# Optimization experiments

Measured on AMD Instinct MI355X. Metric: run time of the kernel, lower is better.

## Reference

```python
import jax, jax.numpy as jnp
import numpy as np
import math

SCALE = math.sqrt(256.0)

def setup_inputs() -> dict:
    key = jax.random.key(0)
    k1, k2, k3, k4, k5 = jax.random.split(key, 5)
    B, C, T, D = 8, 80, 2048, 256
    bound = 1.0 / math.sqrt(C)
    x = jax.random.normal(k1, (B, C, T), dtype=jnp.float32)
    Wk = jax.random.uniform(k2, (D, C), minval=-bound, maxval=bound, dtype=jnp.float32)
    bk = jax.random.uniform(k3, (D,), minval=-bound, maxval=bound, dtype=jnp.float32)
    Wq = jax.random.uniform(k4, (D, C), minval=-bound, maxval=bound, dtype=jnp.float32)
    bq = jax.random.uniform(k5, (D,), minval=-bound, maxval=bound, dtype=jnp.float32)
    return {"x": x, "Wk": Wk, "bk": bk, "Wq": Wq, "bq": bq}

def reference(x, Wk, bk, Wq, bq):
    # x: [B, C=80, T]; work in time-major layout [B, T, C]
    xt = jnp.swapaxes(x, 1, 2)                      # [B, T, C]
    K = xt @ Wk.T + bk                              # [B, T, 256]
    Q = xt @ Wq.T + bq                              # [B, T, 256]
    # softmax over last dim (dim=2 in torch) of K Q^T / sqrt(256)
    att = jax.nn.softmax(jnp.einsum('bid,bjd->bij', K, Q) / SCALE, axis=2)
    # original per-timestep loop is exactly att @ xt (values = raw input, no V proj)
    out = jnp.einsum('bij,bjc->bic', att, xt)       # [B, T, C]
    return jnp.swapaxes(out, 1, 2)                  # [B, C, T]
```

## Files before the change

kernel.cpp:

```cpp
#include <hip/hip_runtime.h>
#include <hip/hip_bf16.h>
#include <math.h>

typedef __bf16 bf16;
typedef __bf16 bf16x8 __attribute__((ext_vector_type(8)));
typedef float  f32x4  __attribute__((ext_vector_type(4)));
typedef float  f32x16 __attribute__((ext_vector_type(16)));
typedef uint32_t u32x2 __attribute__((ext_vector_type(2)));
typedef uint32_t u32x4 __attribute__((ext_vector_type(4)));

#define MFMA16(a, b, c) __builtin_amdgcn_mfma_f32_16x16x32_bf16((a), (b), (c), 0, 0, 0)
#define MFMA32(a, b, c) __builtin_amdgcn_mfma_f32_32x32x16_bf16((a), (b), (c), 0, 0, 0)

typedef const uint32_t __attribute__((address_space(1)))* gq_t;
typedef uint32_t __attribute__((address_space(3)))* lq_t;

constexpr int B_ = 8, C_ = 80, T_ = 2048, D_ = 256;
constexpr int NS = 4;
constexpr float LOG2E_16 = 0.090169989f;

static __device__ inline uint32_t pkbf(float lo, float hi) {
  bf16 l = (bf16)lo, h = (bf16)hi;
  uint16_t lb = __builtin_bit_cast(uint16_t, l), hb = __builtin_bit_cast(uint16_t, h);
  return (uint32_t)lb | ((uint32_t)hb << 16);
}

constexpr int VF_TILE = 3 * 2 * 2 * 32 * 8;

__global__ __launch_bounds__(256) void wconv_kernel(
    const float* __restrict__ Wk, const float* __restrict__ bk,
    const float* __restrict__ Wq, const float* __restrict__ bq,
    bf16* __restrict__ Wbf)
{
  const int mat = blockIdx.x, c8 = blockIdx.y, d = threadIdx.x;
  const float* W    = mat ? Wq : Wk;
  const float* bias = mat ? bq : bk;
  bf16x8 o;
  #pragma unroll
  for (int e = 0; e < 8; ++e) {
    int c = c8 * 8 + e;
    float v = (c < 80) ? W[d * C_ + c] : (c == 80 ? bias[d] : 0.f);
    o[e] = (bf16)v;
  }
  *reinterpret_cast<bf16x8*>(Wbf + (size_t)(mat * 256 + d) * 96 + c8 * 8) = o;
}

__global__ __launch_bounds__(256) void proj_kernel(
    const float* __restrict__ x,
    const bf16* __restrict__ Wbf,
    bf16* __restrict__ Kb,
    bf16* __restrict__ Qb,
    bf16* __restrict__ Vf)
{
  const int t0   = blockIdx.x * 32;
  const int b    = blockIdx.y;
  const int mat  = blockIdx.z;
  const int tid  = threadIdx.x;
  const int w    = tid >> 6;
  const int lane = tid & 63;
  const int h    = lane >> 4;
  const int lr   = lane & 15;

  const float* xb = x + (size_t)b * C_ * T_;

  if (mat == 0) {
    bf16* vout = Vf + (size_t)(b * 64 + blockIdx.x) * VF_TILE;
    #pragma unroll
    for (int g = 0; g < 2; ++g) {
      int f = tid + g * 256;
      if (f < 384) {
        int il2 = f & 31, hi2 = (f >> 5) & 1, kj2 = (f >> 6) & 1, cb2 = f >> 7;
        int c = cb2 * 32 + il2;
        bf16x8 o;
        if (c < 80) {
          const float* sp = xb + (size_t)c * T_ + t0 + kj2 * 16 + hi2 * 8;
          f32x4 v0 = *reinterpret_cast<const f32x4*>(sp);
          f32x4 v1 = *reinterpret_cast<const f32x4*>(sp + 4);
          #pragma unroll
          for (int e = 0; e < 4; ++e) { o[e] = (bf16)v0[e]; o[e + 4] = (bf16)v1[e]; }
        } else {
          #pragma unroll
          for (int e = 0; e < 8; ++e) o[e] = (bf16)0.f;
        }
        *reinterpret_cast<bf16x8*>(vout + f * 8) = o;
      }
    }
  }

  bf16x8 afrag[2][3];
  #pragma unroll
  for (int ib = 0; ib < 2; ++ib) {
    int t = t0 + ib * 16 + lr;
    #pragma unroll
    for (int ks = 0; ks < 3; ++ks) {
      bf16x8 v;
      #pragma unroll
      for (int e = 0; e < 8; ++e) {
        int c = ks * 32 + h * 8 + e;
        float val;
        if (c < 80)       val = xb[c * T_ + t];
        else if (c == 80) val = 1.0f;
        else              val = 0.0f;
        v[e] = (bf16)val;
      }
      afrag[ib][ks] = v;
    }
  }

  const int nb0 = w * 4;
  bf16* outp = mat ? Qb : Kb;

  f32x4 acc[2][4];
  #pragma unroll
  for (int ib = 0; ib < 2; ++ib)
    #pragma unroll
    for (int nb = 0; nb < 4; ++nb)
      acc[ib][nb] = f32x4{0.f, 0.f, 0.f, 0.f};

  #pragma unroll
  for (int nb = 0; nb < 4; ++nb) {
    int d = (nb0 + nb) * 16 + lr;
    const bf16* wrow = Wbf + (size_t)(mat * 256 + d) * 96;
    #pragma unroll
    for (int ks = 0; ks < 3; ++ks) {
      bf16x8 bv = *reinterpret_cast<const bf16x8*>(wrow + ks * 32 + h * 8);
      #pragma unroll
      for (int ib = 0; ib < 2; ++ib)
        acc[ib][nb] = MFMA16(afrag[ib][ks], bv, acc[ib][nb]);
    }
  }

  #pragma unroll
  for (int ib = 0; ib < 2; ++ib)
    #pragma unroll
    for (int nb = 0; nb < 4; ++nb) {
      int d = (nb0 + nb) * 16 + lr;
      #pragma unroll
      for (int r = 0; r < 4; ++r) {
        int t = t0 + ib * 16 + h * 4 + r;
        outp[(size_t)(b * T_ + t) * D_ + d] = (bf16)acc[ib][nb][r];
      }
    }
}

__global__ __launch_bounds__(256, 2) void attn_kernel(
    const bf16* __restrict__ Kb,
    const bf16* __restrict__ Qb,
    const bf16* __restrict__ Vf,
    float* __restrict__ Opart,
    float* __restrict__ mpart,
    float* __restrict__ lpart)
{
  constexpr int BN = 64, NSTG = T_ / BN;
  constexpr int STG_PER = NSTG / NS;
  __shared__ bf16 qlds[2][BN * D_];

  const int flat = blockIdx.x;
  const int b    = flat & 7;
  const int rem  = flat >> 3;
  const int it   = rem & 15;
  const int s    = rem >> 4;
  const int i0   = it * 128;

  const int tid  = threadIdx.x;
  const int w    = tid >> 6;
  const int lane = tid & 63;
  const int il   = lane & 31;
  const int hi   = lane >> 5;
  const int iw   = i0 + w * 32;

  const bf16* Kbase = Kb + (size_t)b * T_ * D_;
  const bf16* Qbase = Qb + (size_t)b * T_ * D_;
  const bf16* Vbase = Vf + (size_t)b * 64 * VF_TILE;

  bf16x8 kf[16];
  {
    const bf16* kp = Kbase + (size_t)(iw + il) * D_ + hi * 8;
    #pragma unroll
    for (int ks = 0; ks < 16; ++ks)
      kf[ks] = *reinterpret_cast<const bf16x8*>(kp + ks * 16);
  }

  f32x16 oacc[3];
  #pragma unroll
  for (int cb = 0; cb < 3; ++cb)
    #pragma unroll
    for (int r = 0; r < 16; ++r) oacc[cb][r] = 0.f;
  float m_run = -INFINITY, l_run = 0.f;

  const int st0 = s * STG_PER;
  const int off = (it & 3) * 2;
  auto smap = [&](int t) { return st0 + ((t - st0 + off) & (STG_PER - 1)); };

  auto stage = [&](int st, int buf) {
    #pragma unroll
    for (int q = 0; q < 8; ++q) {
      int f = tid + 256 * q;
      int j = f >> 5, c = f & 31;
      const bf16* src = Qbase + (size_t)(st * BN + j) * D_ + ((c ^ (j & 31)) << 3);
      __builtin_amdgcn_global_load_lds((gq_t)src,
          (lq_t)&qlds[buf][(q * 256 + w * 64) * 8], 16, 0, 0);
    }
  };

  stage(smap(st0), 0);
  asm volatile("s_waitcnt vmcnt(0)" ::: "memory");
  __syncthreads();

  int cur = 0;
  for (int t = st0; t < st0 + STG_PER; ++t, cur ^= 1) {
    const int st = smap(t);
    if (t + 1 < st0 + STG_PER) stage(smap(t + 1), cur ^ 1);

    #pragma unroll
    for (int hf = 0; hf < 2; ++hf) {
      const int j32 = st * 2 + hf;

      const bf16* vt = Vbase + (size_t)j32 * VF_TILE + lane * 8;
      bf16x8 vf[3][2];
      #pragma unroll
      for (int cb = 0; cb < 3; ++cb)
        #pragma unroll
        for (int kj = 0; kj < 2; ++kj)
          vf[cb][kj] = *reinterpret_cast<const bf16x8*>(vt + (cb * 2 + kj) * 512);

      f32x16 sacc;
      #pragma unroll
      for (int r = 0; r < 16; ++r) sacc[r] = 0.f;
      __builtin_amdgcn_s_setprio(1);
      #pragma unroll
      for (int ks = 0; ks < 16; ++ks) {
        bf16x8 qa = *reinterpret_cast<const bf16x8*>(
            &qlds[cur][(hf * 32 + il) * 256 + (((hi + 2 * ks) ^ il) << 3)]);
        sacc = MFMA32(qa, kf[ks], sacc);
      }
      __builtin_amdgcn_s_setprio(0);

      float p16[16];
      #pragma unroll
      for (int r = 0; r < 16; ++r) p16[r] = sacc[r];
      float q0 = fmaxf(fmaxf(p16[0],  p16[1]),  p16[2]);
      float q1 = fmaxf(fmaxf(p16[3],  p16[4]),  p16[5]);
      float q2 = fmaxf(fmaxf(p16[6],  p16[7]),  p16[8]);
      float q3 = fmaxf(fmaxf(p16[9],  p16[10]), p16[11]);
      float q4 = fmaxf(fmaxf(p16[12], p16[13]), p16[14]);
      float mx = fmaxf(fmaxf(fmaxf(q0, q1), q2),
                       fmaxf(fmaxf(q3, q4), p16[15]));
      mx = fmaxf(mx, __shfl_xor(mx, 32));

      if (!__all(mx <= m_run + 48.f)) {
        float mnew  = fmaxf(m_run, mx);
        float alpha = exp2f((m_run - mnew) * LOG2E_16);
        m_run = mnew;
        l_run *= alpha;
        #pragma unroll
        for (int cb = 0; cb < 3; ++cb)
          #pragma unroll
          for (int r = 0; r < 16; ++r) oacc[cb][r] *= alpha;
      }
      #pragma unroll
      for (int r = 0; r < 16; ++r)
        p16[r] = exp2f((p16[r] - m_run) * LOG2E_16);
      {
        float s0 = (p16[0] + p16[1]) + (p16[2] + p16[3]);
        float s1 = (p16[4] + p16[5]) + (p16[6] + p16[7]);
        float s2 = (p16[8] + p16[9]) + (p16[10] + p16[11]);
        float s3 = (p16[12] + p16[13]) + (p16[14] + p16[15]);
        l_run += (s0 + s1) + (s2 + s3);
      }

      uint32_t a0 = pkbf(p16[0],  p16[1]),  a1 = pkbf(p16[2],  p16[3]);
      uint32_t c0 = pkbf(p16[4],  p16[5]),  c1 = pkbf(p16[6],  p16[7]);
      uint32_t a2 = pkbf(p16[8],  p16[9]),  a3 = pkbf(p16[10], p16[11]);
      uint32_t c2 = pkbf(p16[12], p16[13]), c3 = pkbf(p16[14], p16[15]);
      u32x2 w0 = __builtin_amdgcn_permlane32_swap(a0, c0, false, false);
      u32x2 w1 = __builtin_amdgcn_permlane32_swap(a1, c1, false, false);
      u32x2 w2 = __builtin_amdgcn_permlane32_swap(a2, c2, false, false);
      u32x2 w3 = __builtin_amdgcn_permlane32_swap(a3, c3, false, false);
      u32x4 pb0 = { w0[0], w1[0], w0[1], w1[1] };
      u32x4 pb1 = { w2[0], w3[0], w2[1], w3[1] };
      bf16x8 pbf0 = __builtin_bit_cast(bf16x8, pb0);
      bf16x8 pbf1 = __builtin_bit_cast(bf16x8, pb1);

      __builtin_amdgcn_s_setprio(1);
      #pragma unroll
      for (int cb = 0; cb < 3; ++cb) {
        oacc[cb] = MFMA32(vf[cb][0], pbf0, oacc[cb]);
        oacc[cb] = MFMA32(vf[cb][1], pbf1, oacc[cb]);
      }
      __builtin_amdgcn_s_setprio(0);
    }

    asm volatile("s_waitcnt vmcnt(0)" ::: "memory");
    __syncthreads();
  }

  l_run += __shfl_xor(l_run, 32);

  float* ob = Opart + (size_t)(s * B_ + b) * C_ * T_;
  #pragma unroll
  for (int cb = 0; cb < 3; ++cb)
    #pragma unroll
    for (int r = 0; r < 16; ++r) {
      if (cb < 2 || r < 8) {
        int c = cb * 32 + (r & 3) + 8 * (r >> 2) + 4 * hi;
        ob[(size_t)c * T_ + iw + il] = oacc[cb][r];
      }
    }
  if (lane < 32) {
    mpart[(size_t)(s * B_ + b) * T_ + iw + il] = m_run;
    lpart[(size_t)(s * B_ + b) * T_ + iw + il] = l_run;
  }
}

__global__ __launch_bounds__(256) void merge_kernel(
    const float* __restrict__ Opart,
    const float* __restrict__ mpart,
    const float* __restrict__ lpart,
    float* __restrict__ out)
{
  const int b      = blockIdx.y;
  const int tid    = threadIdx.x;
  const int slot   = tid & 15;
  const int cstrip = tid >> 4;
  const int t4     = blockIdx.x * 64 + slot * 4;

  f32x4 m[NS], e[NS];
  f32x4 mmax;
  #pragma unroll
  for (int s2 = 0; s2 < NS; ++s2)
    m[s2] = *reinterpret_cast<const f32x4*>(&mpart[(size_t)(s2 * B_ + b) * T_ + t4]);
  #pragma unroll
  for (int r = 0; r < 4; ++r) {
    mmax[r] = m[0][r];
    #pragma unroll
    for (int s2 = 1; s2 < NS; ++s2) mmax[r] = fmaxf(mmax[r], m[s2][r]);
  }
  f32x4 lsum = f32x4{0.f, 0.f, 0.f, 0.f};
  #pragma unroll
  for (int s2 = 0; s2 < NS; ++s2) {
    f32x4 lv = *reinterpret_cast<const f32x4*>(&lpart[(size_t)(s2 * B_ + b) * T_ + t4]);
    #pragma unroll
    for (int r = 0; r < 4; ++r) e[s2][r] = exp2f((m[s2][r] - mmax[r]) * LOG2E_16);
    lsum += e[s2] * lv;
  }
  f32x4 inv;
  #pragma unroll
  for (int r = 0; r < 4; ++r) inv[r] = 1.0f / lsum[r];

  #pragma unroll
  for (int cc = 0; cc < 5; ++cc) {
    const int c = cstrip * 5 + cc;
    f32x4 acc = f32x4{0.f, 0.f, 0.f, 0.f};
    #pragma unroll
    for (int s2 = 0; s2 < NS; ++s2)
      acc += *reinterpret_cast<const f32x4*>(
                 &Opart[((size_t)(s2 * B_ + b) * C_ + c) * T_ + t4]) * e[s2];
    *reinterpret_cast<f32x4*>(&out[((size_t)b * C_ + c) * T_ + t4]) = acc * inv;
  }
}

extern "C" void kernel_launch(void* const* d_in, const int* in_sizes, int n_in,
                              void* d_out, int out_size, void* d_ws, size_t ws_size,
                              hipStream_t stream) {
  (void)in_sizes; (void)n_in; (void)out_size; (void)ws_size;
  const float* x  = (const float*)d_in[0];
  const float* Wk = (const float*)d_in[1];
  const float* bk = (const float*)d_in[2];
  const float* Wq = (const float*)d_in[3];
  const float* bq = (const float*)d_in[4];
  float* out = (float*)d_out;

  char* ws = (char*)d_ws;
  const size_t MB = 1024 * 1024;
  bf16*  Kb    = (bf16*)(ws);
  bf16*  Qb    = (bf16*)(ws + 8 * MB);
  bf16*  Vf    = (bf16*)(ws + 16 * MB);
  bf16*  Wbf   = (bf16*)(ws + 19 * MB);
  float* Opart = (float*)(ws + 20 * MB);
  float* mpart = (float*)(ws + 42 * MB);
  float* lpart = (float*)(ws + 43 * MB);

  dim3 blk(256);
  wconv_kernel<<<dim3(2, 12), blk, 0, stream>>>(Wk, bk, Wq, bq, Wbf);
  dim3 g1(T_ / 32, B_, 2);
  proj_kernel<<<g1, blk, 0, stream>>>(x, Wbf, Kb, Qb, Vf);
  attn_kernel<<<dim3(16 * NS * B_), blk, 0, stream>>>(Kb, Qb, Vf, Opart, mpart, lpart);
  dim3 g3(T_ / 64, B_);
  merge_kernel<<<g3, blk, 0, stream>>>(Opart, mpart, lpart, out);
}
```

Baseline: 62.51 us.

## Fuse split-K merge into attention kernel via last-block atomic counter

Removes the separate merge kernel launch. Each attention block bumps an atomic counter for its (batch, query tile) after writing its partial output and its m and l values. The last of the NS split blocks to arrive does the log-sum-exp merge for that 128-row tile. This saves a kernel launch and some tail latency, at the cost of a memset launch, a threadfence and serialized merge work inside the tail blocks.

```diff
diff --git a/kernel.cpp b/kernel.cpp
--- a/kernel.cpp
+++ b/kernel.cpp
@@ -149,11 +149,14 @@
     const bf16* __restrict__ Vf,
     float* __restrict__ Opart,
     float* __restrict__ mpart,
-    float* __restrict__ lpart)
+    float* __restrict__ lpart,
+    int*   __restrict__ cnt,
+    float* __restrict__ out)
 {
   constexpr int BN = 64, NSTG = T_ / BN;
   constexpr int STG_PER = NSTG / NS;
   __shared__ bf16 qlds[2][BN * D_];
+  __shared__ int lastflag;
 
   const int flat = blockIdx.x;
   const int b    = flat & 7;
@@ -311,52 +314,50 @@
     mpart[(size_t)(s * B_ + b) * T_ + iw + il] = m_run;
     lpart[(size_t)(s * B_ + b) * T_ + iw + il] = l_run;
   }
-}
-
-__global__ __launch_bounds__(256) void merge_kernel(
-    const float* __restrict__ Opart,
-    const float* __restrict__ mpart,
-    const float* __restrict__ lpart,
-    float* __restrict__ out)
-{
-  const int b      = blockIdx.y;
-  const int tid    = threadIdx.x;
-  const int slot   = tid & 15;
-  const int cstrip = tid >> 4;
-  const int t4     = blockIdx.x * 64 + slot * 4;
-
-  f32x4 m[NS], e[NS];
-  f32x4 mmax;
-  #pragma unroll
-  for (int s2 = 0; s2 < NS; ++s2)
-    m[s2] = *reinterpret_cast<const f32x4*>(&mpart[(size_t)(s2 * B_ + b) * T_ + t4]);
-  #pragma unroll
-  for (int r = 0; r < 4; ++r) {
-    mmax[r] = m[0][r];
-    #pragma unroll
-    for (int s2 = 1; s2 < NS; ++s2) mmax[r] = fmaxf(mmax[r], m[s2][r]);
-  }
-  f32x4 lsum = f32x4{0.f, 0.f, 0.f, 0.f};
-  #pragma unroll
-  for (int s2 = 0; s2 < NS; ++s2) {
-    f32x4 lv = *reinterpret_cast<const f32x4*>(&lpart[(size_t)(s2 * B_ + b) * T_ + t4]);
-    #pragma unroll
-    for (int r = 0; r < 4; ++r) e[s2][r] = exp2f((m[s2][r] - mmax[r]) * LOG2E_16);
-    lsum += e[s2] * lv;
-  }
-  f32x4 inv;
-  #pragma unroll
-  for (int r = 0; r < 4; ++r) inv[r] = 1.0f / lsum[r];
-
-  #pragma unroll
-  for (int cc = 0; cc < 5; ++cc) {
-    const int c = cstrip * 5 + cc;
-    f32x4 acc = f32x4{0.f, 0.f, 0.f, 0.f};
+
+  __threadfence();
+  __syncthreads();
+  if (tid == 0)
+    lastflag = (atomicAdd(&cnt[b * 16 + it], 1) == NS - 1);
+  __syncthreads();
+  if (lastflag) {
+    const int slot = tid & 31;
+    const int cs   = tid >> 5;
+    const int t4   = i0 + slot * 4;
+
+    f32x4 mm[NS], ee[NS];
+    f32x4 mmax;
     #pragma unroll
     for (int s2 = 0; s2 < NS; ++s2)
-      acc += *reinterpret_cast<const f32x4*>(
-                 &Opart[((size_t)(s2 * B_ + b) * C_ + c) * T_ + t4]) * e[s2];
-    *reinterpret_cast<f32x4*>(&out[((size_t)b * C_ + c) * T_ + t4]) = acc * inv;
+      mm[s2] = *reinterpret_cast<const f32x4*>(&mpart[(size_t)(s2 * B_ + b) * T_ + t4]);
+    #pragma unroll
+    for (int r = 0; r < 4; ++r) {
+      mmax[r] = mm[0][r];
+      #pragma unroll
+      for (int s2 = 1; s2 < NS; ++s2) mmax[r] = fmaxf(mmax[r], mm[s2][r]);
+    }
+    f32x4 lsum = f32x4{0.f, 0.f, 0.f, 0.f};
+    #pragma unroll
+    for (int s2 = 0; s2 < NS; ++s2) {
+      f32x4 lv = *reinterpret_cast<const f32x4*>(&lpart[(size_t)(s2 * B_ + b) * T_ + t4]);
+      #pragma unroll
+      for (int r = 0; r < 4; ++r) ee[s2][r] = exp2f((mm[s2][r] - mmax[r]) * LOG2E_16);
+      lsum += ee[s2] * lv;
+    }
+    f32x4 inv;
+    #pragma unroll
+    for (int r = 0; r < 4; ++r) inv[r] = 1.0f / lsum[r];
+
+    #pragma unroll
+    for (int k = 0; k < 10; ++k) {
+      const int c = cs * 10 + k;
+      f32x4 acc = f32x4{0.f, 0.f, 0.f, 0.f};
+      #pragma unroll
+      for (int s2 = 0; s2 < NS; ++s2)
+        acc += *reinterpret_cast<const f32x4*>(
+                   &Opart[((size_t)(s2 * B_ + b) * C_ + c) * T_ + t4]) * ee[s2];
+      *reinterpret_cast<f32x4*>(&out[((size_t)b * C_ + c) * T_ + t4]) = acc * inv;
+    }
   }
 }
 
@@ -380,12 +381,14 @@
   float* Opart = (float*)(ws + 20 * MB);
   float* mpart = (float*)(ws + 42 * MB);
   float* lpart = (float*)(ws + 43 * MB);
+  int*   cnt   = (int*)(ws + 44 * MB);
+
+  hipMemsetAsync(cnt, 0, B_ * 16 * sizeof(int), stream);
 
   dim3 blk(256);
   wconv_kernel<<<dim3(2, 12), blk, 0, stream>>>(Wk, bk, Wq, bq, Wbf);
   dim3 g1(T_ / 32, B_, 2);
   proj_kernel<<<g1, blk, 0, stream>>>(x, Wbf, Kb, Qb, Vf);
-  attn_kernel<<<dim3(16 * NS * B_), blk, 0, stream>>>(Kb, Qb, Vf, Opart, mpart, lpart);
-  dim3 g3(T_ / 64, B_);
-  merge_kernel<<<g3, blk, 0, stream>>>(Opart, mpart, lpart, out);
-}
+  attn_kernel<<<dim3(16 * NS * B_), blk, 0, stream>>>(Kb, Qb, Vf, Opart, mpart,
+                                                      lpart, cnt, out);
+}
```

After: 112.8 us. 80.4% more time.

## Switch attention to 16x16 MFMA tiles with 64-row blocks and tighter V padding

Applied to the files above, without the earlier changes.

Rewrites the attention kernel to use 16x16x32 MFMAs, with each wave owning 16 query rows and each block 64 rows over 32-column Q stages. The grid doubles and launch bounds allow three blocks per CU. V fragments are repacked into 5 blocks of 16 channels instead of 3 blocks of 32, removing the zero-padded channels 80-95. The change trades extra K reloads and more frequent softmax and sync steps for more parallelism, lower per-thread register use and less padded MFMA work.

```diff
diff --git a/kernel.cpp b/kernel.cpp
--- a/kernel.cpp
+++ b/kernel.cpp
@@ -5,12 +5,10 @@
 typedef __bf16 bf16;
 typedef __bf16 bf16x8 __attribute__((ext_vector_type(8)));
 typedef float  f32x4  __attribute__((ext_vector_type(4)));
-typedef float  f32x16 __attribute__((ext_vector_type(16)));
 typedef uint32_t u32x2 __attribute__((ext_vector_type(2)));
 typedef uint32_t u32x4 __attribute__((ext_vector_type(4)));
 
 #define MFMA16(a, b, c) __builtin_amdgcn_mfma_f32_16x16x32_bf16((a), (b), (c), 0, 0, 0)
-#define MFMA32(a, b, c) __builtin_amdgcn_mfma_f32_32x32x16_bf16((a), (b), (c), 0, 0, 0)
 
 typedef const uint32_t __attribute__((address_space(1)))* gq_t;
 typedef uint32_t __attribute__((address_space(3)))* lq_t;
@@ -25,7 +23,7 @@
   return (uint32_t)lb | ((uint32_t)hb << 16);
 }
 
-constexpr int VF_TILE = 3 * 2 * 2 * 32 * 8;
+constexpr int VF_TILE = 5 * 64 * 8;
 
 __global__ __launch_bounds__(256) void wconv_kernel(
     const float* __restrict__ Wk, const float* __restrict__ bk,
@@ -68,20 +66,15 @@
     #pragma unroll
     for (int g = 0; g < 2; ++g) {
       int f = tid + g * 256;
-      if (f < 384) {
-        int il2 = f & 31, hi2 = (f >> 5) & 1, kj2 = (f >> 6) & 1, cb2 = f >> 7;
-        int c = cb2 * 32 + il2;
+      if (f < 320) {
+        int l2 = f & 63, cb2 = f >> 6;
+        int c = cb2 * 16 + (l2 & 15);
+        const float* sp = xb + (size_t)c * T_ + t0 + ((l2 >> 4) << 3);
+        f32x4 v0 = *reinterpret_cast<const f32x4*>(sp);
+        f32x4 v1 = *reinterpret_cast<const f32x4*>(sp + 4);
         bf16x8 o;
-        if (c < 80) {
-          const float* sp = xb + (size_t)c * T_ + t0 + kj2 * 16 + hi2 * 8;
-          f32x4 v0 = *reinterpret_cast<const f32x4*>(sp);
-          f32x4 v1 = *reinterpret_cast<const f32x4*>(sp + 4);
-          #pragma unroll
-          for (int e = 0; e < 4; ++e) { o[e] = (bf16)v0[e]; o[e + 4] = (bf16)v1[e]; }
-        } else {
-          #pragma unroll
-          for (int e = 0; e < 8; ++e) o[e] = (bf16)0.f;
-        }
+        #pragma unroll
+        for (int e = 0; e < 4; ++e) { o[e] = (bf16)v0[e]; o[e + 4] = (bf16)v1[e]; }
         *reinterpret_cast<bf16x8*>(vout + f * 8) = o;
       }
     }
@@ -143,7 +136,7 @@
     }
 }
 
-__global__ __launch_bounds__(256, 2) void attn_kernel(
+__global__ __launch_bounds__(256, 3) void attn_kernel(
     const bf16* __restrict__ Kb,
     const bf16* __restrict__ Qb,
     const bf16* __restrict__ Vf,
@@ -151,53 +144,51 @@
     float* __restrict__ mpart,
     float* __restrict__ lpart)
 {
-  constexpr int BN = 64, NSTG = T_ / BN;
+  constexpr int BN = 32, NSTG = T_ / BN;
   constexpr int STG_PER = NSTG / NS;
   __shared__ bf16 qlds[2][BN * D_];
 
   const int flat = blockIdx.x;
   const int b    = flat & 7;
   const int rem  = flat >> 3;
-  const int it   = rem & 15;
-  const int s    = rem >> 4;
-  const int i0   = it * 128;
+  const int it   = rem & 31;
+  const int s    = rem >> 5;
+  const int i0   = it * 64;
 
   const int tid  = threadIdx.x;
   const int w    = tid >> 6;
   const int lane = tid & 63;
-  const int il   = lane & 31;
-  const int hi   = lane >> 5;
-  const int iw   = i0 + w * 32;
+  const int li   = lane & 15;
+  const int g    = lane >> 4;
+  const int iw   = i0 + w * 16;
 
   const bf16* Kbase = Kb + (size_t)b * T_ * D_;
   const bf16* Qbase = Qb + (size_t)b * T_ * D_;
   const bf16* Vbase = Vf + (size_t)b * 64 * VF_TILE;
 
-  bf16x8 kf[16];
+  bf16x8 kf[8];
   {
-    const bf16* kp = Kbase + (size_t)(iw + il) * D_ + hi * 8;
-    #pragma unroll
-    for (int ks = 0; ks < 16; ++ks)
-      kf[ks] = *reinterpret_cast<const bf16x8*>(kp + ks * 16);
-  }
-
-  f32x16 oacc[3];
-  #pragma unroll
-  for (int cb = 0; cb < 3; ++cb)
-    #pragma unroll
-    for (int r = 0; r < 16; ++r) oacc[cb][r] = 0.f;
+    const bf16* kp = Kbase + (size_t)(iw + li) * D_ + g * 8;
+    #pragma unroll
+    for (int ks = 0; ks < 8; ++ks)
+      kf[ks] = *reinterpret_cast<const bf16x8*>(kp + ks * 32);
+  }
+
+  f32x4 oacc[5];
+  #pragma unroll
+  for (int cb = 0; cb < 5; ++cb) oacc[cb] = f32x4{0.f, 0.f, 0.f, 0.f};
   float m_run = -INFINITY, l_run = 0.f;
 
   const int st0 = s * STG_PER;
-  const int off = (it & 3) * 2;
+  const int off = it & 15;
   auto smap = [&](int t) { return st0 + ((t - st0 + off) & (STG_PER - 1)); };
 
   auto stage = [&](int st, int buf) {
     #pragma unroll
-    for (int q = 0; q < 8; ++q) {
+    for (int q = 0; q < 4; ++q) {
       int f = tid + 256 * q;
       int j = f >> 5, c = f & 31;
-      const bf16* src = Qbase + (size_t)(st * BN + j) * D_ + ((c ^ (j & 31)) << 3);
+      const bf16* src = Qbase + (size_t)(st * BN + j) * D_ + ((c ^ j) << 3);
       __builtin_amdgcn_global_load_lds((gq_t)src,
           (lq_t)&qlds[buf][(q * 256 + w * 64) * 8], 16, 0, 0);
     }
@@ -212,104 +203,84 @@
     const int st = smap(t);
     if (t + 1 < st0 + STG_PER) stage(smap(t + 1), cur ^ 1);
 
-    #pragma unroll
-    for (int hf = 0; hf < 2; ++hf) {
-      const int j32 = st * 2 + hf;
-
-      const bf16* vt = Vbase + (size_t)j32 * VF_TILE + lane * 8;
-      bf16x8 vf[3][2];
+    const bf16* vt = Vbase + (size_t)st * VF_TILE + lane * 8;
+    bf16x8 vf[5];
+    #pragma unroll
+    for (int cb = 0; cb < 5; ++cb)
+      vf[cb] = *reinterpret_cast<const bf16x8*>(vt + cb * 512);
+
+    f32x4 sacc_a = f32x4{0.f, 0.f, 0.f, 0.f};
+    f32x4 sacc_b = f32x4{0.f, 0.f, 0.f, 0.f};
+    __builtin_amdgcn_s_setprio(1);
+    #pragma unroll
+    for (int ks = 0; ks < 8; ++ks) {
+      const int chunk = ks * 4 + g;
+      bf16x8 qa0 = *reinterpret_cast<const bf16x8*>(
+          &qlds[cur][li * 256 + ((chunk ^ li) << 3)]);
+      bf16x8 qa1 = *reinterpret_cast<const bf16x8*>(
+          &qlds[cur][(16 + li) * 256 + ((chunk ^ (16 + li)) << 3)]);
+      sacc_a = MFMA16(qa0, kf[ks], sacc_a);
+      sacc_b = MFMA16(qa1, kf[ks], sacc_b);
+    }
+    __builtin_amdgcn_s_setprio(0);
+
+    float p8[8];
+    #pragma unroll
+    for (int r = 0; r < 4; ++r) { p8[r] = sacc_a[r]; p8[4 + r] = sacc_b[r]; }
+    float mx = fmaxf(fmaxf(fmaxf(p8[0], p8[1]), fmaxf(p8[2], p8[3])),
+                     fmaxf(fmaxf(p8[4], p8[5]), fmaxf(p8[6], p8[7])));
+    mx = fmaxf(mx, __shfl_xor(mx, 16));
+    mx = fmaxf(mx, __shfl_xor(mx, 32));
+
+    if (!__all(mx <= m_run + 48.f)) {
+      float mnew  = fmaxf(m_run, mx);
+      float alpha = exp2f((m_run - mnew) * LOG2E_16);
+      m_run = mnew;
+      l_run *= alpha;
       #pragma unroll
-      for (int cb = 0; cb < 3; ++cb)
+      for (int cb = 0; cb < 5; ++cb)
         #pragma unroll
-        for (int kj = 0; kj < 2; ++kj)
-          vf[cb][kj] = *reinterpret_cast<const bf16x8*>(vt + (cb * 2 + kj) * 512);
-
-      f32x16 sacc;
-      #pragma unroll
-      for (int r = 0; r < 16; ++r) sacc[r] = 0.f;
-      __builtin_amdgcn_s_setprio(1);
-      #pragma unroll
-      for (int ks = 0; ks < 16; ++ks) {
-        bf16x8 qa = *reinterpret_cast<const bf16x8*>(
-            &qlds[cur][(hf * 32 + il) * 256 + (((hi + 2 * ks) ^ il) << 3)]);
-        sacc = MFMA32(qa, kf[ks], sacc);
-      }
-      __builtin_amdgcn_s_setprio(0);
-
-      float p16[16];
-      #pragma unroll
-      for (int r = 0; r < 16; ++r) p16[r] = sacc[r];
-      float q0 = fmaxf(fmaxf(p16[0],  p16[1]),  p16[2]);
-      float q1 = fmaxf(fmaxf(p16[3],  p16[4]),  p16[5]);
-      float q2 = fmaxf(fmaxf(p16[6],  p16[7]),  p16[8]);
-      float q3 = fmaxf(fmaxf(p16[9],  p16[10]), p16[11]);
-      float q4 = fmaxf(fmaxf(p16[12], p16[13]), p16[14]);
-      float mx = fmaxf(fmaxf(fmaxf(q0, q1), q2),
-                       fmaxf(fmaxf(q3, q4), p16[15]));
-      mx = fmaxf(mx, __shfl_xor(mx, 32));
-
-      if (!__all(mx <= m_run + 48.f)) {
-        float mnew  = fmaxf(m_run, mx);
-        float alpha = exp2f((m_run - mnew) * LOG2E_16);
-        m_run = mnew;
-        l_run *= alpha;
-        #pragma unroll
-        for (int cb = 0; cb < 3; ++cb)
-          #pragma unroll
-          for (int r = 0; r < 16; ++r) oacc[cb][r] *= alpha;
-      }
-      #pragma unroll
-      for (int r = 0; r < 16; ++r)
-        p16[r] = exp2f((p16[r] - m_run) * LOG2E_16);
-      {
-        float s0 = (p16[0] + p16[1]) + (p16[2] + p16[3]);
-        float s1 = (p16[4] + p16[5]) + (p16[6] + p16[7]);
-        float s2 = (p16[8] + p16[9]) + (p16[10] + p16[11]);
-        float s3 = (p16[12] + p16[13]) + (p16[14] + p16[15]);
-        l_run += (s0 + s1) + (s2 + s3);
-      }
-
-      uint32_t a0 = pkbf(p16[0],  p16[1]),  a1 = pkbf(p16[2],  p16[3]);
-      uint32_t c0 = pkbf(p16[4],  p16[5]),  c1 = pkbf(p16[6],  p16[7]);
-      uint32_t a2 = pkbf(p16[8],  p16[9]),  a3 = pkbf(p16[10], p16[11]);
-      uint32_t c2 = pkbf(p16[12], p16[13]), c3 = pkbf(p16[14], p16[15]);
-      u32x2 w0 = __builtin_amdgcn_permlane32_swap(a0, c0, false, false);
-      u32x2 w1 = __builtin_amdgcn_permlane32_swap(a1, c1, false, false);
-      u32x2 w2 = __builtin_amdgcn_permlane32_swap(a2, c2, false, false);
-      u32x2 w3 = __builtin_amdgcn_permlane32_swap(a3, c3, false, false);
-      u32x4 pb0 = { w0[0], w1[0], w0[1], w1[1] };
-      u32x4 pb1 = { w2[0], w3[0], w2[1], w3[1] };
-      bf16x8 pbf0 = __builtin_bit_cast(bf16x8, pb0);
-      bf16x8 pbf1 = __builtin_bit_cast(bf16x8, pb1);
-
-      __builtin_amdgcn_s_setprio(1);
-      #pragma unroll
-      for (int cb = 0; cb < 3; ++cb) {
-        oacc[cb] = MFMA32(vf[cb][0], pbf0, oacc[cb]);
-        oacc[cb] = MFMA32(vf[cb][1], pbf1, oacc[cb]);
-      }
-      __builtin_amdgcn_s_setprio(0);
-    }
+        for (int r = 0; r < 4; ++r) oacc[cb][r] *= alpha;
+    }
+    #pragma unroll
+    for (int r = 0; r < 8; ++r)
+      p8[r] = exp2f((p8[r] - m_run) * LOG2E_16);
+    l_run += ((p8[0] + p8[1]) + (p8[2] + p8[3])) +
+             ((p8[4] + p8[5]) + (p8[6] + p8[7]));
+
+    uint32_t A0 = pkbf(p8[0], p8[1]), A1 = pkbf(p8[2], p8[3]);
+    uint32_t B0 = pkbf(p8[4], p8[5]), B1 = pkbf(p8[6], p8[7]);
+    u32x2 sw0 = __builtin_amdgcn_permlane32_swap(A0, B0, false, false);
+    u32x2 tw0 = __builtin_amdgcn_permlane16_swap(sw0[0], sw0[1], false, false);
+    u32x2 sw1 = __builtin_amdgcn_permlane32_swap(A1, B1, false, false);
+    u32x2 tw1 = __builtin_amdgcn_permlane16_swap(sw1[0], sw1[1], false, false);
+    u32x4 pb = { tw0[0], tw1[0], tw0[1], tw1[1] };
+    bf16x8 pbf = __builtin_bit_cast(bf16x8, pb);
+
+    __builtin_amdgcn_s_setprio(1);
+    #pragma unroll
+    for (int cb = 0; cb < 5; ++cb)
+      oacc[cb] = MFMA16(vf[cb], pbf, oacc[cb]);
+    __builtin_amdgcn_s_setprio(0);
 
     asm volatile("s_waitcnt vmcnt(0)" ::: "memory");
     __syncthreads();
   }
 
+  l_run += __shfl_xor(l_run, 16);
   l_run += __shfl_xor(l_run, 32);
 
   float* ob = Opart + (size_t)(s * B_ + b) * C_ * T_;
   #pragma unroll
-  for (int cb = 0; cb < 3; ++cb)
-    #pragma unroll
-    for (int r = 0; r < 16; ++r) {
-      if (cb < 2 || r < 8) {
-        int c = cb * 32 + (r & 3) + 8 * (r >> 2) + 4 * hi;
-        ob[(size_t)c * T_ + iw + il] = oacc[cb][r];
-      }
-    }
-  if (lane < 32) {
-    mpart[(size_t)(s * B_ + b) * T_ + iw + il] = m_run;
-    lpart[(size_t)(s * B_ + b) * T_ + iw + il] = l_run;
+  for (int cb = 0; cb < 5; ++cb)
+    #pragma unroll
+    for (int r = 0; r < 4; ++r) {
+      int c = cb * 16 + g * 4 + r;
+      ob[(size_t)c * T_ + iw + li] = oacc[cb][r];
+    }
+  if (lane < 16) {
+    mpart[(size_t)(s * B_ + b) * T_ + iw + lane] = m_run;
+    lpart[(size_t)(s * B_ + b) * T_ + iw + lane] = l_run;
   }
 }
 
@@ -385,7 +356,7 @@
   wconv_kernel<<<dim3(2, 12), blk, 0, stream>>>(Wk, bk, Wq, bq, Wbf);
   dim3 g1(T_ / 32, B_, 2);
   proj_kernel<<<g1, blk, 0, stream>>>(x, Wbf, Kb, Qb, Vf);
-  attn_kernel<<<dim3(16 * NS * B_), blk, 0, stream>>>(Kb, Qb, Vf, Opart, mpart, lpart);
+  attn_kernel<<<dim3(32 * NS * B_), blk, 0, stream>>>(Kb, Qb, Vf, Opart, mpart, lpart);
   dim3 g3(T_ / 64, B_);
   merge_kernel<<<g3, blk, 0, stream>>>(Opart, mpart, lpart, out);
 }
```

Result: slower. 72.38 us (+15.8%).
